# Kernel optimization log

Hardware: AMD Instinct MI355X
Metric: run time of the kernel (lower is better)

The kernel has to match this reference:

```python
import jax, jax.numpy as jnp
import numpy as np

# 27-neighbor permutation used by the original module: columns are (depth, height, width)
# offsets within the 3x3x3 window (0..2), center at (1,1,1).
INDICES = np.array([
    [2, 0, 0], [2, 0, 1], [2, 0, 2], [1, 0, 2], [0, 0, 2], [0, 0, 1], [0, 0, 0], [1, 0, 0], [1, 0, 1],
    [2, 1, 0], [2, 1, 1], [2, 1, 2], [1, 1, 2], [0, 1, 2], [0, 1, 1], [0, 1, 0], [1, 1, 0],
    [2, 2, 0], [2, 2, 1], [2, 2, 2], [1, 2, 2], [0, 2, 2], [0, 2, 1], [0, 2, 0], [1, 2, 0], [1, 2, 1],
    [1, 1, 1]], dtype=np.int64)

# Positions (into the permuted 27-vector) whose product defines erosion for each connectivity.
VOX = {
    6:  [8, 10, 12, 25, 16, 14, 26],
    18: [8, 10, 12, 25, 16, 14, 1, 3, 5, 7, 9, 11, 13, 15, 18, 20, 22, 24, 26],
    26: [8, 10, 12, 25, 16, 14, 1, 3, 5, 7, 9, 11, 13, 15, 18, 20, 22, 24, 0, 2, 4, 6, 17, 19, 21, 23, 26],
}


def soft_erosion_3d(im, iterations, connectivity):
    """im: [B, C, D, H, W] in [0,1]. Product-of-neighbors soft erosion, padded with 1."""
    offs = INDICES[np.asarray(VOX[int(connectivity)])]  # [K, 3] static offsets
    D, H, W = im.shape[2], im.shape[3], im.shape[4]
    for _ in range(int(iterations)):
        p = jnp.pad(im, ((0, 0), (0, 0), (1, 1), (1, 1), (1, 1)), constant_values=1.0)
        prod = None
        for a, b, c in offs:  # fixed small set of shifted views -> fused product stencil
            s = p[:, :, a:a + D, b:b + H, c:c + W]
            prod = s if prod is None else prod * s
        im = im * prod
    return im


def setup_inputs() -> dict:
    key = jax.random.key(0)
    im = jax.random.uniform(key, (2, 1, 256, 256, 256), dtype=jnp.float32)
    return {"im": im, "iterations": 2, "connectivity": 6}


def reference(im, iterations, connectivity):
    return soft_erosion_3d(im, iterations, connectivity)
```

## Files before the change

### kernel.cpp

```cpp
#include <hip/hip_runtime.h>


#define DD 256
#define HH 256
#define HW 65536
#define DT 16

typedef float nfloat4 __attribute__((ext_vector_type(4)));

__device__ __forceinline__ float wleft(float x) {
    float v = __shfl_up(x, 1, 64);
    return ((threadIdx.x & 63) == 0) ? 1.0f : v;
}
__device__ __forceinline__ float wright(float x) {
    float v = __shfl_down(x, 1, 64);
    return ((threadIdx.x & 63) == 63) ? 1.0f : v;
}
__device__ __forceinline__ float4 f4mul(float4 a, float4 b) {
    a.x *= b.x; a.y *= b.y; a.z *= b.z; a.w *= b.w; return a;
}
__device__ __forceinline__ float4 i1core(float4 c) {
    float lw = wleft(c.w), rw = wright(c.x);
    float4 r;
    r.x = c.x * c.x * (lw  * c.y);
    r.y = c.y * c.y * (c.x * c.z);
    r.z = c.z * c.z * (c.y * c.w);
    r.w = c.w * c.w * (c.z * rw);
    return r;
}
__device__ __forceinline__ int dcl(int d) { return d < 0 ? 0 : (d > DD - 1 ? DD - 1 : d); }

__global__ __launch_bounds__(256) void erode6_fused(const float* __restrict__ in,
                                                    float* __restrict__ out) {
    const int bx  = blockIdx.x;
    const int swz = (bx & 7) * 128 + (bx >> 3);

    const int cc = threadIdx.x & 63;
    const int wv = __builtin_amdgcn_readfirstlane((int)(threadIdx.x >> 6));

    const int hblk = swz & 31;
    const int dchk = (swz >> 5) & 15;
    const int b    = swz >> 9;

    const int h = hblk * 8 + wv * 2;
    const int S = dchk * DT;

    const bool vbU = (h >= 1);
    const bool voU = (h >= 2);
    const bool vbD = (h + 2 <= HH - 1);
    const bool voD = (h + 3 <= HH - 1);
    const int rowU  = vbU ? h - 1 : 0;
    const int rowOU = voU ? h - 2 : 0;
    const int rowD  = vbD ? h + 2 : HH - 1;
    const int rowOD = voD ? h + 3 : HH - 1;

    const float* __restrict__ ip = in  + (size_t)b * (DD * HW);
    float* __restrict__       op = out + (size_t)b * (DD * HW);

    const float* pC0 = ip + (h     << 8) + (cc << 2);
    const float* pC1 = ip + ((h+1) << 8) + (cc << 2);
    const float* pBU = ip + (rowU  << 8) + (cc << 2);
    const float* pBD = ip + (rowD  << 8) + (cc << 2);
    const float* pOU = ip + (rowOU << 8) + (cc << 2);
    const float* pOD = ip + (rowOD << 8) + (cc << 2);
    float* pO0 = op + (h << 8) + (cc << 2);

#define LD(p, pl) (*reinterpret_cast<const float4*>((p) + ((pl) << 16)))

    const int Sm1 = S >= 1 ? S - 1 : 0;
    const int Sm2 = S >= 2 ? S - 2 : 0;

    float4 c0_m2 = LD(pC0, Sm2), c0_m1 = LD(pC0, Sm1);
    float4 c0_t  = LD(pC0, S), c0_t1 = LD(pC0, S + 1), c0_t2 = LD(pC0, S + 2);
    float4 c1_m2 = LD(pC1, Sm2), c1_m1 = LD(pC1, Sm1);
    float4 c1_t  = LD(pC1, S), c1_t1 = LD(pC1, S + 1), c1_t2 = LD(pC1, S + 2);
    float4 bu_m = LD(pBU, Sm1), bu_c = LD(pBU, S), bu_p = LD(pBU, S + 1);
    float4 bd_m = LD(pBD, Sm1), bd_c = LD(pBD, S), bd_p = LD(pBD, S + 1);
    float4 ou = LD(pOU, S), od = LD(pOD, S);

    float4 i0_m = i1core(c0_m1);
    i0_m = f4mul(i0_m, c0_t);
    if (S >= 2) i0_m = f4mul(i0_m, c0_m2);
    if (vbU)    i0_m = f4mul(i0_m, bu_m);
    i0_m = f4mul(i0_m, c1_m1);

    float4 i1_m = i1core(c1_m1);
    i1_m = f4mul(i1_m, c1_t);
    if (S >= 2) i1_m = f4mul(i1_m, c1_m2);
    i1_m = f4mul(i1_m, c0_m1);
    if (vbD)    i1_m = f4mul(i1_m, bd_m);

    float4 i0_c = i1core(c0_t);
    if (S >= 1) i0_c = f4mul(i0_c, c0_m1);
    i0_c = f4mul(i0_c, c0_t1);
    if (vbU)    i0_c = f4mul(i0_c, bu_c);
    i0_c = f4mul(i0_c, c1_t);

    float4 i1_c = i1core(c1_t);
    if (S >= 1) i1_c = f4mul(i1_c, c1_m1);
    i1_c = f4mul(i1_c, c1_t1);
    i1_c = f4mul(i1_c, c0_t);
    if (vbD)    i1_c = f4mul(i1_c, bd_c);

#pragma unroll
    for (int k = 0; k < DT; ++k) {
        const int t = S + k;

        float4 pf_c0 = LD(pC0, dcl(t + 3)), pf_c1 = LD(pC1, dcl(t + 3));
        float4 pf_bu = LD(pBU, dcl(t + 2)), pf_bd = LD(pBD, dcl(t + 2));
        float4 pf_ou = LD(pOU, dcl(t + 1)), pf_od = LD(pOD, dcl(t + 1));

        const bool fm  = (t > 0);
        const bool fp  = (t < DD - 1);
        const bool fD2 = (t < DD - 2);

        float4 IbU = {1.f, 1.f, 1.f, 1.f};
        if (vbU) {
            IbU = i1core(bu_c);
            if (fm)  IbU = f4mul(IbU, bu_m);
            if (fp)  IbU = f4mul(IbU, bu_p);
            if (voU) IbU = f4mul(IbU, ou);
            IbU = f4mul(IbU, c0_t);
        }
        float4 IbD = {1.f, 1.f, 1.f, 1.f};
        if (vbD) {
            IbD = i1core(bd_c);
            if (fm)  IbD = f4mul(IbD, bd_m);
            if (fp)  IbD = f4mul(IbD, bd_p);
            IbD = f4mul(IbD, c1_t);
            if (voD) IbD = f4mul(IbD, od);
        }

        float4 i0_p = i1core(c0_t1);
        i0_p = f4mul(i0_p, c0_t);
        if (fD2) i0_p = f4mul(i0_p, c0_t2);
        if (vbU) i0_p = f4mul(i0_p, bu_p);
        i0_p = f4mul(i0_p, c1_t1);

        float4 i1_p = i1core(c1_t1);
        i1_p = f4mul(i1_p, c1_t);
        if (fD2) i1_p = f4mul(i1_p, c1_t2);
        i1_p = f4mul(i1_p, c0_t1);
        if (vbD) i1_p = f4mul(i1_p, bd_p);

        float4 o0 = i1core(i0_c);
        if (fm) o0 = f4mul(o0, i0_m);
        if (fp) o0 = f4mul(o0, i0_p);
        o0 = f4mul(o0, IbU);
        o0 = f4mul(o0, i1_c);

        float4 o1 = i1core(i1_c);
        if (fm) o1 = f4mul(o1, i1_m);
        if (fp) o1 = f4mul(o1, i1_p);
        o1 = f4mul(o1, i0_c);
        o1 = f4mul(o1, IbD);

        nfloat4 v0 = {o0.x, o0.y, o0.z, o0.w};
        nfloat4 v1 = {o1.x, o1.y, o1.z, o1.w};
        __builtin_nontemporal_store(v0, reinterpret_cast<nfloat4*>(pO0 + (t << 16)));
        __builtin_nontemporal_store(v1, reinterpret_cast<nfloat4*>(pO0 + (t << 16) + 256));

        i0_m = i0_c; i0_c = i0_p; i1_m = i1_c; i1_c = i1_p;
        c0_t = c0_t1; c0_t1 = c0_t2; c0_t2 = pf_c0;
        c1_t = c1_t1; c1_t1 = c1_t2; c1_t2 = pf_c1;
        bu_m = bu_c; bu_c = bu_p; bu_p = pf_bu;
        bd_m = bd_c; bd_c = bd_p; bd_p = pf_bd;
        ou = pf_ou; od = pf_od;
    }
#undef LD
}

extern "C" void kernel_launch(void* const* d_in, const int* in_sizes, int n_in,
                              void* d_out, int out_size, void* d_ws, size_t ws_size,
                              hipStream_t stream) {
    const float* in  = (const float*)d_in[0];
    float*       out = (float*)d_out;

    dim3 block(256);
    dim3 grid(1024);
    erode6_fused<<<grid, block, 0, stream>>>(in, out);
}
```

Baseline: 47.42 us.

## Swap stencil axes: stream along H rows and split D planes across waves

The kernel now marches along the H axis in the register-rotating sliding window and assigns depth planes to waves, where before it marched along D and assigned H rows. Consecutive loads and stores per step are now 1 KB apart within a plane instead of 256 KB apart across planes, which should improve DRAM page and cache locality. Halo planes are now neighbouring depth planes. Halo reuse between blocks via L2 changes, since neighbouring blocks now share planes rather than rows.

```diff
diff --git a/kernel.cpp b/kernel.cpp
--- a/kernel.cpp
+++ b/kernel.cpp
@@ -4,7 +4,7 @@
 #define DD 256
 #define HH 256
 #define HW 65536
-#define DT 16
+#define HT 16
 
 typedef float nfloat4 __attribute__((ext_vector_type(4)));
 
@@ -28,7 +28,7 @@
     r.w = c.w * c.w * (c.z * rw);
     return r;
 }
-__device__ __forceinline__ int dcl(int d) { return d < 0 ? 0 : (d > DD - 1 ? DD - 1 : d); }
+__device__ __forceinline__ int hcl(int r) { return r < 0 ? 0 : (r > HH - 1 ? HH - 1 : r); }
 
 __global__ __launch_bounds__(256) void erode6_fused(const float* __restrict__ in,
                                                     float* __restrict__ out) {
@@ -38,34 +38,34 @@
     const int cc = threadIdx.x & 63;
     const int wv = __builtin_amdgcn_readfirstlane((int)(threadIdx.x >> 6));
 
-    const int hblk = swz & 31;
-    const int dchk = (swz >> 5) & 15;
+    const int pblk = swz & 31;
+    const int hchk = (swz >> 5) & 15;
     const int b    = swz >> 9;
 
-    const int h = hblk * 8 + wv * 2;
-    const int S = dchk * DT;
+    const int p = pblk * 8 + wv * 2;
+    const int S = hchk * HT;
 
-    const bool vbU = (h >= 1);
-    const bool voU = (h >= 2);
-    const bool vbD = (h + 2 <= HH - 1);
-    const bool voD = (h + 3 <= HH - 1);
-    const int rowU  = vbU ? h - 1 : 0;
-    const int rowOU = voU ? h - 2 : 0;
-    const int rowD  = vbD ? h + 2 : HH - 1;
-    const int rowOD = voD ? h + 3 : HH - 1;
+    const bool vbU = (p >= 1);
+    const bool voU = (p >= 2);
+    const bool vbD = (p + 2 <= DD - 1);
+    const bool voD = (p + 3 <= DD - 1);
+    const int plU  = vbU ? p - 1 : 0;
+    const int plOU = voU ? p - 2 : 0;
+    const int plD  = vbD ? p + 2 : DD - 1;
+    const int plOD = voD ? p + 3 : DD - 1;
 
     const float* __restrict__ ip = in  + (size_t)b * (DD * HW);
     float* __restrict__       op = out + (size_t)b * (DD * HW);
 
-    const float* pC0 = ip + (h     << 8) + (cc << 2);
-    const float* pC1 = ip + ((h+1) << 8) + (cc << 2);
-    const float* pBU = ip + (rowU  << 8) + (cc << 2);
-    const float* pBD = ip + (rowD  << 8) + (cc << 2);
-    const float* pOU = ip + (rowOU << 8) + (cc << 2);
-    const float* pOD = ip + (rowOD << 8) + (cc << 2);
-    float* pO0 = op + (h << 8) + (cc << 2);
+    const float* pC0 = ip + (p     << 16) + (cc << 2);
+    const float* pC1 = ip + ((p+1) << 16) + (cc << 2);
+    const float* pBU = ip + (plU   << 16) + (cc << 2);
+    const float* pBD = ip + (plD   << 16) + (cc << 2);
+    const float* pOU = ip + (plOU  << 16) + (cc << 2);
+    const float* pOD = ip + (plOD  << 16) + (cc << 2);
+    float* pO0 = op + (p << 16) + (cc << 2);
 
-#define LD(p, pl) (*reinterpret_cast<const float4*>((p) + ((pl) << 16)))
+#define LD(q, r) (*reinterpret_cast<const float4*>((q) + ((r) << 8)))
 
     const int Sm1 = S >= 1 ? S - 1 : 0;
     const int Sm2 = S >= 2 ? S - 2 : 0;
@@ -103,16 +103,16 @@
     if (vbD)    i1_c = f4mul(i1_c, bd_c);
 
 #pragma unroll
-    for (int k = 0; k < DT; ++k) {
+    for (int k = 0; k < HT; ++k) {
         const int t = S + k;
 
-        float4 pf_c0 = LD(pC0, dcl(t + 3)), pf_c1 = LD(pC1, dcl(t + 3));
-        float4 pf_bu = LD(pBU, dcl(t + 2)), pf_bd = LD(pBD, dcl(t + 2));
-        float4 pf_ou = LD(pOU, dcl(t + 1)), pf_od = LD(pOD, dcl(t + 1));
+        float4 pf_c0 = LD(pC0, hcl(t + 3)), pf_c1 = LD(pC1, hcl(t + 3));
+        float4 pf_bu = LD(pBU, hcl(t + 2)), pf_bd = LD(pBD, hcl(t + 2));
+        float4 pf_ou = LD(pOU, hcl(t + 1)), pf_od = LD(pOD, hcl(t + 1));
 
         const bool fm  = (t > 0);
-        const bool fp  = (t < DD - 1);
-        const bool fD2 = (t < DD - 2);
+        const bool fp  = (t < HH - 1);
+        const bool fD2 = (t < HH - 2);
 
         float4 IbU = {1.f, 1.f, 1.f, 1.f};
         if (vbU) {
@@ -157,8 +157,8 @@
 
         nfloat4 v0 = {o0.x, o0.y, o0.z, o0.w};
         nfloat4 v1 = {o1.x, o1.y, o1.z, o1.w};
-        __builtin_nontemporal_store(v0, reinterpret_cast<nfloat4*>(pO0 + (t << 16)));
-        __builtin_nontemporal_store(v1, reinterpret_cast<nfloat4*>(pO0 + (t << 16) + 256));
+        __builtin_nontemporal_store(v0, reinterpret_cast<nfloat4*>(pO0 + (t << 8)));
+        __builtin_nontemporal_store(v1, reinterpret_cast<nfloat4*>(pO0 + (t << 8) + HW));
 
         i0_m = i0_c; i0_c = i0_p; i1_m = i1_c; i1_c = i1_p;
         c0_t = c0_t1; c0_t1 = c0_t2; c0_t2 = pf_c0;
```

Measured after the change: 51.32 us. +8.2%, slower.
